# Kernel tuning notes

Hardware: AMD Instinct MI355X
Metric: run time of the kernel (lower is better)

The kernel has to match this reference:

```python
import jax, jax.numpy as jnp
import numpy as np

N_NODES = 100000
N_EDGES = 1600000
IN_FEATS, HIDDEN, OUT_MU, OUT_LV = 256, 128, 64, 64


def setup_inputs() -> dict:
    key = jax.random.key(0)
    ks = jax.random.split(key, 8)
    X = jax.random.normal(ks[0], (N_NODES, IN_FEATS), dtype=jnp.float32)
    edge_index = jax.random.randint(ks[1], (2, N_EDGES), 0, N_NODES, dtype=jnp.int64)
    def glorot(k, shape):
        lim = np.sqrt(6.0 / (shape[0] + shape[1])).astype(np.float32)
        return jax.random.uniform(k, shape, jnp.float32, -lim, lim)
    W1 = glorot(ks[2], (IN_FEATS, HIDDEN))
    b1 = jnp.zeros((HIDDEN,), jnp.float32)
    Wmu = glorot(ks[3], (HIDDEN, OUT_MU))
    bmu = jnp.zeros((OUT_MU,), jnp.float32)
    Wlv = glorot(ks[4], (HIDDEN, OUT_LV))
    blv = jnp.zeros((OUT_LV,), jnp.float32)
    return {"X": X, "edge_index": edge_index, "W1": W1, "b1": b1,
            "Wmu": Wmu, "bmu": bmu, "Wlv": Wlv, "blv": blv}


def _gcn_norm(edge_index, num_nodes):
    # Add self-loops (PyG GCNConv default) and compute symmetric normalization.
    loop = jnp.arange(num_nodes, dtype=edge_index.dtype)
    row = jnp.concatenate([edge_index[0], loop])  # source
    col = jnp.concatenate([edge_index[1], loop])  # target
    deg = jax.ops.segment_sum(jnp.ones_like(col, dtype=jnp.float32), col,
                              num_segments=num_nodes)
    dinv = jnp.where(deg > 0, jax.lax.rsqrt(deg), 0.0)
    norm = dinv[row] * dinv[col]  # [E+N]
    return row, col, norm


def _gcn_conv(x, W, b, row, col, norm, num_nodes):
    # Linear transform, then normalized sparse neighbor aggregation at targets.
    h = x @ W                                   # [N, F_out]
    msg = h[row] * norm[:, None]                # gather + scale, [E+N, F_out]
    out = jax.ops.segment_sum(msg, col, num_segments=num_nodes)
    return out + b


def reference(X, edge_index, W1, b1, Wmu, bmu, Wlv, blv):
    n = X.shape[0]
    row, col, norm = _gcn_norm(edge_index, n)
    H = jax.nn.relu(_gcn_conv(X, W1, b1, row, col, norm, n))
    mu = _gcn_conv(H, Wmu, bmu, row, col, norm, n)
    lv = _gcn_conv(H, Wlv, blv, row, col, norm, n)
    return (mu, lv)
```

## Files before the change

### kernel.cpp

```cpp
#include <hip/hip_runtime.h>
#include <hip/hip_bf16.h>
#include <cstdint>

#define N_FEATS_IN 256
#define HID 128
#define OUTF 64
#define NBMAX 400
#define BCAP 6144

typedef __bf16 bf16x8 __attribute__((ext_vector_type(8)));
typedef __bf16 bf16x4 __attribute__((ext_vector_type(4)));
typedef __bf16 bf16x2 __attribute__((ext_vector_type(2)));
typedef float f32x4 __attribute__((ext_vector_type(4)));



__global__ __launch_bounds__(256) void bucket_count(const int* __restrict__ ei, int E,
    int CH, int NB, int* __restrict__ gbk, int* __restrict__ bbase) {
  __shared__ int cnt[NBMAX];
  const int t = threadIdx.x, blk = blockIdx.x;
  for (int i = t; i < NB; i += 256) cnt[i] = 0;
  __syncthreads();
  int base = blk * CH, lim = min(base + CH, E);
  for (int i = base + t; i < lim; i += 256) atomicAdd(&cnt[ei[E + i] >> 8], 1);
  __syncthreads();
  for (int i = t; i < NB; i += 256) {
    int b = (i + blk) % NB;
    int v = cnt[b];
    bbase[(size_t)blk * NB + b] = (v > 0) ? atomicAdd(&gbk[b], v) : 0;
  }
}

__global__ __launch_bounds__(512) void bucket_scan(const int* __restrict__ gbk,
    int* __restrict__ gbkoff, int NB, int E) {
  __shared__ int ts[512];
  const int t = threadIdx.x;
  int v = (t < NB) ? gbk[t] : 0;
  ts[t] = v;
  __syncthreads();
  for (int off = 1; off < 512; off <<= 1) {
    int u = (t >= off) ? ts[t - off] : 0;
    __syncthreads();
    ts[t] += u;
    __syncthreads();
  }
  if (t < NB) gbkoff[t] = ts[t] - v;
  if (t == 0) gbkoff[NB] = E;
}

__global__ __launch_bounds__(256) void bucket_scatter(const int* __restrict__ ei, int E,
    int CH, int NB, const int* __restrict__ gbkoff, const int* __restrict__ bbase,
    int2* __restrict__ bucketed) {
  __shared__ int cur[NBMAX];
  const int t = threadIdx.x, blk = blockIdx.x;
  for (int i = t; i < NB; i += 256)
    cur[i] = gbkoff[i] + bbase[(size_t)blk * NB + i];
  __syncthreads();
  int base = blk * CH, lim = min(base + CH, E);
  for (int i = base + t; i < lim; i += 256) {
    int s = ei[i];
    int c = ei[E + i];
    int p = atomicAdd(&cur[c >> 8], 1);
    bucketed[p] = make_int2(s, c);
  }
}

__global__ __launch_bounds__(256) void bucket_csr(const int2* __restrict__ bucketed,
    const int* __restrict__ gbkoff, int NB, int N, int E,
    float* __restrict__ dinv, int* __restrict__ ptr, int* __restrict__ csrc) {
  __shared__ int2 eb[BCAP];
  __shared__ int cnt[256], scn[256], cur[256];
  const int b = blockIdx.x, t = threadIdx.x;
  const int beg = gbkoff[b], end = gbkoff[b + 1];
  const int M = end - beg;
  cnt[t] = 0;
  __syncthreads();
  const bool inlds = (M <= BCAP);
  if (inlds) {
    for (int i = t; i < M; i += 256) {
      int2 r = bucketed[beg + i];
      eb[i] = r;
      atomicAdd(&cnt[r.y & 255], 1);
    }
  } else {
    for (int i = t; i < M; i += 256) atomicAdd(&cnt[bucketed[beg + i].y & 255], 1);
  }
  __syncthreads();
  const int c0 = cnt[t];
  scn[t] = c0;
  __syncthreads();
  for (int off = 1; off < 256; off <<= 1) {
    int u = (t >= off) ? scn[t - off] : 0;
    __syncthreads();
    scn[t] += u;
    __syncthreads();
  }
  const int excl = scn[t] - c0;
  const int node = b * 256 + t;
  if (node < N) {
    ptr[node] = beg + excl;
    dinv[node] = rsqrtf((float)(c0 + 1));
  }
  if (b == NB - 1 && t == 0) ptr[N] = E;
  cur[t] = excl;
  __syncthreads();
  if (inlds) {
    for (int i = t; i < M; i += 256) {
      int2 r = eb[i];
      int slot = atomicAdd(&cur[r.y & 255], 1);
      csrc[beg + slot] = r.x;
    }
  } else {
    for (int i = t; i < M; i += 256) {
      int2 r = bucketed[beg + i];
      int slot = atomicAdd(&cur[r.y & 255], 1);
      csrc[beg + slot] = r.x;
    }
  }
}


__global__ __launch_bounds__(256) void pack_all_kernel(const float* __restrict__ W1,
    const float* __restrict__ Wmu, const float* __restrict__ Wlv,
    __bf16* __restrict__ W1p, __bf16* __restrict__ Wcp) {
  int idx = blockIdx.x * 256 + threadIdx.x;
  if (idx < 32768) {
    int j = idx & 7, l = (idx >> 3) & 63, t = (idx >> 9) & 7, s = idx >> 12;
    int k = s * 32 + (l >> 4) * 8 + j;
    int n = t * 16 + (l & 15);
    W1p[idx] = (__bf16)W1[k * HID + n];
  } else if (idx < 49152) {
    int i2 = idx - 32768;
    int j = i2 & 7, l = (i2 >> 3) & 63, t = (i2 >> 9) & 7, s = i2 >> 12;
    int k = s * 32 + (l >> 4) * 8 + j;
    int g = t * 16 + (l & 15);
    float v = (g < OUTF) ? Wmu[k * OUTF + g] : Wlv[k * OUTF + (g - OUTF)];
    Wcp[i2] = (__bf16)v;
  }
}


__global__ __launch_bounds__(256) void gemm1_mfma(const float* __restrict__ X,
    const __bf16* __restrict__ Wp, const float* __restrict__ dinv,
    __bf16* __restrict__ Yb, int nrows) {
  const int tid = threadIdx.x;
  const int lane = tid & 63;
  const int wave = tid >> 6;
  const int lm = lane & 15;
  const int q = lane >> 4;
  const int rowbase = blockIdx.x * 128 + wave * 32;

  const int r0 = min(rowbase + lm, nrows - 1);
  const int r1 = min(rowbase + 16 + lm, nrows - 1);
  const float* x0 = X + (size_t)r0 * N_FEATS_IN + q * 8;
  const float* x1 = X + (size_t)r1 * N_FEATS_IN + q * 8;

  const bf16x8* wp = (const bf16x8*)Wp;

  f32x4 acc[2][8];
#pragma unroll
  for (int m = 0; m < 2; ++m)
#pragma unroll
    for (int t = 0; t < 8; ++t) acc[m][t] = (f32x4)0.f;

#pragma unroll
  for (int s = 0; s < 8; ++s) {
    float4 l0 = *(const float4*)(x0 + s * 32);
    float4 h0 = *(const float4*)(x0 + s * 32 + 4);
    float4 l1 = *(const float4*)(x1 + s * 32);
    float4 h1 = *(const float4*)(x1 + s * 32 + 4);
    bf16x8 a0, a1;
    a0[0] = (__bf16)l0.x; a0[1] = (__bf16)l0.y; a0[2] = (__bf16)l0.z; a0[3] = (__bf16)l0.w;
    a0[4] = (__bf16)h0.x; a0[5] = (__bf16)h0.y; a0[6] = (__bf16)h0.z; a0[7] = (__bf16)h0.w;
    a1[0] = (__bf16)l1.x; a1[1] = (__bf16)l1.y; a1[2] = (__bf16)l1.z; a1[3] = (__bf16)l1.w;
    a1[4] = (__bf16)h1.x; a1[5] = (__bf16)h1.y; a1[6] = (__bf16)h1.z; a1[7] = (__bf16)h1.w;
#pragma unroll
    for (int t = 0; t < 8; ++t) {
      bf16x8 b = wp[(s * 8 + t) * 64 + lane];
      acc[0][t] = __builtin_amdgcn_mfma_f32_16x16x32_bf16(a0, b, acc[0][t], 0, 0, 0);
      acc[1][t] = __builtin_amdgcn_mfma_f32_16x16x32_bf16(a1, b, acc[1][t], 0, 0, 0);
    }
  }

  float dd[2][4];
#pragma unroll
  for (int m = 0; m < 2; ++m)
#pragma unroll
    for (int r2 = 0; r2 < 4; ++r2) {
      int row = rowbase + m * 16 + q * 4 + r2;
      dd[m][r2] = (row < nrows) ? dinv[row] : 0.f;
    }

#pragma unroll
  for (int m = 0; m < 2; ++m) {
    int rb = rowbase + m * 16 + q * 4;
#pragma unroll
    for (int t = 0; t < 8; ++t) {
      __bf16* yslice = Yb + (size_t)t * nrows * 16;
#pragma unroll
      for (int r2 = 0; r2 < 4; ++r2) {
        int row = rb + r2;
        if (row < nrows)
          yslice[(size_t)row * 16 + lm] = (__bf16)(acc[m][t][r2] * dd[m][r2]);
      }
    }
  }
}


__global__ __launch_bounds__(256) void agg_kernel(const __bf16* __restrict__ Fin,
    const int* __restrict__ ptr, const int* __restrict__ csrc,
    const float* __restrict__ dinv, const float* __restrict__ bias,
    __bf16* __restrict__ Fout, int do_relu, int N) {
  const int tid = threadIdx.x;
  const int s = blockIdx.x & 7;
  const int tb = blockIdx.x >> 3;
  const int g = tid >> 2;
  const int fl = tid & 3;
  const int c = tb * 64 + g;
  if (c >= N) return;

  const __bf16* F = Fin + (size_t)s * N * 16;
  const float d = dinv[c];
  bf16x4 sv = ((const bf16x4*)(F + (size_t)c * 16))[fl];
  float a0 = (float)sv[0], a1 = (float)sv[1], a2 = (float)sv[2], a3 = (float)sv[3];

  const int beg = ptr[c], end = ptr[c + 1];
  int e = beg;
  for (; e + 8 <= end; e += 8) {
    int r[8];
#pragma unroll
    for (int i = 0; i < 8; ++i) r[i] = csrc[e + i];
    bf16x4 v[8];
#pragma unroll
    for (int i = 0; i < 8; ++i) v[i] = ((const bf16x4*)(F + (size_t)r[i] * 16))[fl];
#pragma unroll
    for (int i = 0; i < 8; ++i) {
      a0 += (float)v[i][0];
      a1 += (float)v[i][1];
      a2 += (float)v[i][2];
      a3 += (float)v[i][3];
    }
  }
  for (; e < end; ++e) {
    int r = csrc[e];
    bf16x4 v = ((const bf16x4*)(F + (size_t)r * 16))[fl];
    a0 += (float)v[0];
    a1 += (float)v[1];
    a2 += (float)v[2];
    a3 += (float)v[3];
  }

  if (do_relu) {
    float4 bv = ((const float4*)bias)[s * 4 + fl];
    a0 = fmaxf(fmaf(d, a0, bv.x), 0.f) * d;
    a1 = fmaxf(fmaf(d, a1, bv.y), 0.f) * d;
    a2 = fmaxf(fmaf(d, a2, bv.z), 0.f) * d;
    a3 = fmaxf(fmaf(d, a3, bv.w), 0.f) * d;
  } else {
    a0 *= d; a1 *= d; a2 *= d; a3 *= d;
  }
  bf16x4 o;
  o[0] = (__bf16)a0; o[1] = (__bf16)a1; o[2] = (__bf16)a2; o[3] = (__bf16)a3;
  ((bf16x4*)(Fout + (size_t)s * N * 16 + (size_t)c * 16))[fl] = o;
}


__global__ __launch_bounds__(256) void gemm2_mfma(const __bf16* __restrict__ Gb,
    const __bf16* __restrict__ Wp, const float* __restrict__ bmu,
    const float* __restrict__ blv, float* __restrict__ out, int nrows, int ntiles) {
  __shared__ __bf16 bs[16384];
  const int tid = threadIdx.x;
  {
    const float4* s4 = (const float4*)Wp;
    float4* d4 = (float4*)bs;
#pragma unroll
    for (int i = 0; i < 8; ++i) d4[tid + 256 * i] = s4[tid + 256 * i];
  }
  __syncthreads();
  const int lane = tid & 63;
  const int wave = tid >> 6;
  const int lm = lane & 15;
  const int q = lane >> 4;
  const bf16x8* bsv = (const bf16x8*)bs;

  float bv[8];
  size_t obase[8];
#pragma unroll
  for (int t = 0; t < 8; ++t) {
    int col = t * 16 + lm;
    bv[t] = (col < OUTF) ? bmu[col] : blv[col - OUTF];
    obase[t] = (col < OUTF) ? (size_t)col : ((size_t)nrows * OUTF + (col - OUTF));
  }

  for (int tile = blockIdx.x; tile < ntiles; tile += gridDim.x) {
    const int row0 = tile * 64 + wave * 16;
    const int r = min(row0 + lm, nrows - 1);

    bf16x8 xa[4];
#pragma unroll
    for (int si = 0; si < 4; ++si) {
      int chunk = si * 4 + q;
      xa[si] = *(const bf16x8*)(Gb + (size_t)(chunk >> 1) * nrows * 16 +
                                (size_t)r * 16 + (chunk & 1) * 8);
    }

    f32x4 acc[8];
#pragma unroll
    for (int t = 0; t < 8; ++t) acc[t] = (f32x4)0.f;

#pragma unroll
    for (int si = 0; si < 4; ++si) {
#pragma unroll
      for (int t = 0; t < 8; ++t)
        acc[t] = __builtin_amdgcn_mfma_f32_16x16x32_bf16(xa[si], bsv[(si * 8 + t) * 64 + lane],
                                                         acc[t], 0, 0, 0);
    }
#pragma unroll
    for (int t = 0; t < 8; ++t) {
#pragma unroll
      for (int r2 = 0; r2 < 4; ++r2) {
        int row = row0 + q * 4 + r2;
        if (row < nrows) out[obase[t] + (size_t)row * OUTF] = acc[t][r2] + bv[t];
      }
    }
  }
}


extern "C" void kernel_launch(void* const* d_in, const int* in_sizes, int n_in,
                              void* d_out, int out_size, void* d_ws, size_t ws_size,
                              hipStream_t stream) {
  const float* X   = (const float*)d_in[0];
  const int*   ei  = (const int*)d_in[1];
  const float* W1  = (const float*)d_in[2];
  const float* b1  = (const float*)d_in[3];
  const float* Wmu = (const float*)d_in[4];
  const float* bmu = (const float*)d_in[5];
  const float* Wlv = (const float*)d_in[6];
  const float* blv = (const float*)d_in[7];
  float* out = (float*)d_out;

  const int N = in_sizes[0] / N_FEATS_IN;
  const int E = in_sizes[1] / 2;

  char* ws = (char*)d_ws;
  size_t off = 0;
  auto alloc = [&](size_t bytes) -> void* {
    void* p = ws + off;
    off += (bytes + 255) & ~(size_t)255;
    return p;
  };
  __bf16* Yb   = (__bf16*)alloc((size_t)N * HID * 2);
  __bf16* Hb   = (__bf16*)alloc((size_t)N * HID * 2);
  float* dinv  = (float*)alloc((size_t)N * 4);
  int*   ptr   = (int*)alloc((size_t)(N + 1) * 4);
  int2*  bucketed = (int2*)alloc((size_t)E * 8);
  int*   csrc  = (int*)alloc((size_t)E * 4);
  int*   gbk   = (int*)alloc((size_t)NBMAX * 4);
  int*   gbkoff = (int*)alloc((size_t)(NBMAX + 1) * 4);
  int*   bbase = (int*)alloc((size_t)256 * NBMAX * 4);
  __bf16* W1p  = (__bf16*)alloc(32768 * 2);
  __bf16* Wcp  = (__bf16*)alloc(16384 * 2);
  (void)ws_size; (void)n_in; (void)out_size;

  const int NB = (N + 255) >> 8;
  const int P = 256;
  const int CH = (E + P - 1) / P;

  hipMemsetAsync(gbk, 0, (size_t)NB * 4, stream);
  bucket_count<<<P, 256, 0, stream>>>(ei, E, CH, NB, gbk, bbase);
  bucket_scan<<<1, 512, 0, stream>>>(gbk, gbkoff, NB, E);
  bucket_scatter<<<P, 256, 0, stream>>>(ei, E, CH, NB, gbkoff, bbase, bucketed);
  bucket_csr<<<NB, 256, 0, stream>>>(bucketed, gbkoff, NB, N, E, dinv, ptr, csrc);
  pack_all_kernel<<<192, 256, 0, stream>>>(W1, Wmu, Wlv, W1p, Wcp);

  int g1 = (N + 127) / 128;
  gemm1_mfma<<<g1, 256, 0, stream>>>(X, W1p, dinv, Yb, N);
  int ga = ((N + 63) / 64) * 8;
  agg_kernel<<<ga, 256, 0, stream>>>(Yb, ptr, csrc, dinv, b1, Hb, 1, N);
  agg_kernel<<<ga, 256, 0, stream>>>(Hb, ptr, csrc, dinv, b1, Yb, 0, N);
  int ntiles2 = (N + 63) / 64;
  int g2 = ntiles2 < 768 ? ntiles2 : 768;
  gemm2_mfma<<<g2, 256, 0, stream>>>(Yb, Wcp, bmu, blv, out, N, ntiles2);
}
```

Baseline: 452.4 us.

## Sort nodes by in-degree to balance aggregation warps

Builds a degree-bucketed permutation of nodes (64 bins via a global histogram, scan, and scatter) during CSR construction, and has the aggregation kernels process nodes in that order. Nodes with similar degree then land in the same wavefront, reducing divergence from uneven neighbor loop lengths. In exchange it adds two small kernels, an extra memset, an indirection load per node, and loses the locality of consecutive node indices for the self-feature and output accesses.

After: 531.2 us. 1.17x slower.

```diff
diff --git a/kernel.cpp b/kernel.cpp
--- a/kernel.cpp
+++ b/kernel.cpp
@@ -7,6 +7,7 @@
 #define OUTF 64
 #define NBMAX 400
 #define BCAP 6144
+#define DBINS 64
 
 typedef __bf16 bf16x8 __attribute__((ext_vector_type(8)));
 typedef __bf16 bf16x4 __attribute__((ext_vector_type(4)));
@@ -67,13 +68,16 @@
 
 __global__ __launch_bounds__(256) void bucket_csr(const int2* __restrict__ bucketed,
     const int* __restrict__ gbkoff, int NB, int N, int E,
-    float* __restrict__ dinv, int* __restrict__ ptr, int* __restrict__ csrc) {
+    float* __restrict__ dinv, int* __restrict__ ptr, int* __restrict__ csrc,
+    int* __restrict__ dbing, int* __restrict__ noderank) {
   __shared__ int2 eb[BCAP];
   __shared__ int cnt[256], scn[256], cur[256];
+  __shared__ int dh[DBINS], dbase[DBINS];
   const int b = blockIdx.x, t = threadIdx.x;
   const int beg = gbkoff[b], end = gbkoff[b + 1];
   const int M = end - beg;
   cnt[t] = 0;
+  if (t < DBINS) dh[t] = 0;
   __syncthreads();
   const bool inlds = (M <= BCAP);
   if (inlds) {
@@ -97,13 +101,19 @@
   }
   const int excl = scn[t] - c0;
   const int node = b * 256 + t;
+  int bin = 0, lrk = 0;
   if (node < N) {
     ptr[node] = beg + excl;
     dinv[node] = rsqrtf((float)(c0 + 1));
+    bin = min(c0, DBINS - 1);
+    lrk = atomicAdd(&dh[bin], 1);
   }
   if (b == NB - 1 && t == 0) ptr[N] = E;
   cur[t] = excl;
   __syncthreads();
+  if (t < DBINS) dbase[t] = dh[t] ? atomicAdd(&dbing[t * 32], dh[t]) : 0;
+  __syncthreads();
+  if (node < N) noderank[node] = ((dbase[bin] + lrk) << 6) | bin;
   if (inlds) {
     for (int i = t; i < M; i += 256) {
       int2 r = eb[i];
@@ -116,6 +126,27 @@
       int slot = atomicAdd(&cur[r.y & 255], 1);
       csrc[beg + slot] = r.x;
     }
+  }
+}
+
+__global__ __launch_bounds__(64) void deg_scan(const int* __restrict__ dbing,
+    int* __restrict__ dboff) {
+  int t = threadIdx.x;
+  int v = dbing[t * 32];
+  int x = v;
+  for (int off = 1; off < 64; off <<= 1) {
+    int u = __shfl_up(x, off);
+    if (t >= off) x += u;
+  }
+  dboff[t] = x - v;
+}
+
+__global__ __launch_bounds__(256) void perm_scatter(const int* __restrict__ noderank,
+    const int* __restrict__ dboff, int* __restrict__ perm, int N) {
+  int i = blockIdx.x * 256 + threadIdx.x;
+  if (i < N) {
+    int w = noderank[i];
+    perm[dboff[w & 63] + (w >> 6)] = i;
   }
 }
 
@@ -211,14 +242,16 @@
 __global__ __launch_bounds__(256) void agg_kernel(const __bf16* __restrict__ Fin,
     const int* __restrict__ ptr, const int* __restrict__ csrc,
     const float* __restrict__ dinv, const float* __restrict__ bias,
+    const int* __restrict__ perm,
     __bf16* __restrict__ Fout, int do_relu, int N) {
   const int tid = threadIdx.x;
   const int s = blockIdx.x & 7;
   const int tb = blockIdx.x >> 3;
   const int g = tid >> 2;
   const int fl = tid & 3;
-  const int c = tb * 64 + g;
-  if (c >= N) return;
+  const int idx = tb * 64 + g;
+  if (idx >= N) return;
+  const int c = perm[idx];
 
   const __bf16* F = Fin + (size_t)s * N * 16;
   const float d = dinv[c];
@@ -360,6 +393,10 @@
   int*   gbk   = (int*)alloc((size_t)NBMAX * 4);
   int*   gbkoff = (int*)alloc((size_t)(NBMAX + 1) * 4);
   int*   bbase = (int*)alloc((size_t)256 * NBMAX * 4);
+  int*   dbing = (int*)alloc((size_t)DBINS * 32 * 4);
+  int*   dboff = (int*)alloc((size_t)DBINS * 4);
+  int*   noderank = (int*)alloc((size_t)N * 4);
+  int*   perm  = (int*)alloc((size_t)N * 4);
   __bf16* W1p  = (__bf16*)alloc(32768 * 2);
   __bf16* Wcp  = (__bf16*)alloc(16384 * 2);
   (void)ws_size; (void)n_in; (void)out_size;
@@ -369,17 +406,21 @@
   const int CH = (E + P - 1) / P;
 
   hipMemsetAsync(gbk, 0, (size_t)NB * 4, stream);
+  hipMemsetAsync(dbing, 0, (size_t)DBINS * 32 * 4, stream);
   bucket_count<<<P, 256, 0, stream>>>(ei, E, CH, NB, gbk, bbase);
   bucket_scan<<<1, 512, 0, stream>>>(gbk, gbkoff, NB, E);
   bucket_scatter<<<P, 256, 0, stream>>>(ei, E, CH, NB, gbkoff, bbase, bucketed);
-  bucket_csr<<<NB, 256, 0, stream>>>(bucketed, gbkoff, NB, N, E, dinv, ptr, csrc);
+  bucket_csr<<<NB, 256, 0, stream>>>(bucketed, gbkoff, NB, N, E, dinv, ptr, csrc,
+                                     dbing, noderank);
+  deg_scan<<<1, 64, 0, stream>>>(dbing, dboff);
+  perm_scatter<<<(N + 255) / 256, 256, 0, stream>>>(noderank, dboff, perm, N);
   pack_all_kernel<<<192, 256, 0, stream>>>(W1, Wmu, Wlv, W1p, Wcp);
 
   int g1 = (N + 127) / 128;
   gemm1_mfma<<<g1, 256, 0, stream>>>(X, W1p, dinv, Yb, N);
   int ga = ((N + 63) / 64) * 8;
-  agg_kernel<<<ga, 256, 0, stream>>>(Yb, ptr, csrc, dinv, b1, Hb, 1, N);
-  agg_kernel<<<ga, 256, 0, stream>>>(Hb, ptr, csrc, dinv, b1, Yb, 0, N);
+  agg_kernel<<<ga, 256, 0, stream>>>(Yb, ptr, csrc, dinv, b1, perm, Hb, 1, N);
+  agg_kernel<<<ga, 256, 0, stream>>>(Hb, ptr, csrc, dinv, b1, perm, Yb, 0, N);
   int ntiles2 = (N + 63) / 64;
   int g2 = ntiles2 < 768 ? ntiles2 : 768;
   gemm2_mfma<<<g2, 256, 0, stream>>>(Yb, Wcp, bmu, blv, out, N, ntiles2);
```

## Widen feature slices to 32 and pack bucketed edges into single words

Applied to the files above, without the earlier changes.

The bf16 feature slices move from 8 slices of 16 columns to 4 slices of 32 columns. This is applied consistently in gemm1's store, both aggregation passes and gemm2's load, so each gathered neighbour row becomes a 64-byte contiguous read and the aggregation grid has half as many slice passes. The aggregation now loads the 8 neighbour indices cooperatively, one per lane, and broadcasts them with shuffles instead of every lane reading all 8. Bucketed edges are packed into one 32-bit word (low 8 bits of the target in the top byte, source in the low 24 bits), halving that buffer's traffic. The packing assumes node ids fit in 24 bits.

Measured after the change: 430.1 us. 4.9% less time.

```diff
diff --git a/kernel.cpp b/kernel.cpp
--- a/kernel.cpp
+++ b/kernel.cpp
@@ -10,8 +10,8 @@
 
 typedef __bf16 bf16x8 __attribute__((ext_vector_type(8)));
 typedef __bf16 bf16x4 __attribute__((ext_vector_type(4)));
-typedef __bf16 bf16x2 __attribute__((ext_vector_type(2)));
 typedef float f32x4 __attribute__((ext_vector_type(4)));
+
 
 
 
@@ -50,7 +50,7 @@
 
 __global__ __launch_bounds__(256) void bucket_scatter(const int* __restrict__ ei, int E,
     int CH, int NB, const int* __restrict__ gbkoff, const int* __restrict__ bbase,
-    int2* __restrict__ bucketed) {
+    unsigned int* __restrict__ pk) {
   __shared__ int cur[NBMAX];
   const int t = threadIdx.x, blk = blockIdx.x;
   for (int i = t; i < NB; i += 256)
@@ -58,17 +58,17 @@
   __syncthreads();
   int base = blk * CH, lim = min(base + CH, E);
   for (int i = base + t; i < lim; i += 256) {
-    int s = ei[i];
+    unsigned int s = (unsigned int)ei[i];
     int c = ei[E + i];
     int p = atomicAdd(&cur[c >> 8], 1);
-    bucketed[p] = make_int2(s, c);
-  }
-}
-
-__global__ __launch_bounds__(256) void bucket_csr(const int2* __restrict__ bucketed,
+    pk[p] = ((unsigned int)(c & 255) << 24) | s;
+  }
+}
+
+__global__ __launch_bounds__(256) void bucket_csr(const unsigned int* __restrict__ pk,
     const int* __restrict__ gbkoff, int NB, int N, int E,
     float* __restrict__ dinv, int* __restrict__ ptr, int* __restrict__ csrc) {
-  __shared__ int2 eb[BCAP];
+  __shared__ unsigned int eb[BCAP];
   __shared__ int cnt[256], scn[256], cur[256];
   const int b = blockIdx.x, t = threadIdx.x;
   const int beg = gbkoff[b], end = gbkoff[b + 1];
@@ -78,12 +78,12 @@
   const bool inlds = (M <= BCAP);
   if (inlds) {
     for (int i = t; i < M; i += 256) {
-      int2 r = bucketed[beg + i];
+      unsigned int r = pk[beg + i];
       eb[i] = r;
-      atomicAdd(&cnt[r.y & 255], 1);
+      atomicAdd(&cnt[r >> 24], 1);
     }
   } else {
-    for (int i = t; i < M; i += 256) atomicAdd(&cnt[bucketed[beg + i].y & 255], 1);
+    for (int i = t; i < M; i += 256) atomicAdd(&cnt[pk[beg + i] >> 24], 1);
   }
   __syncthreads();
   const int c0 = cnt[t];
@@ -106,15 +106,15 @@
   __syncthreads();
   if (inlds) {
     for (int i = t; i < M; i += 256) {
-      int2 r = eb[i];
-      int slot = atomicAdd(&cur[r.y & 255], 1);
-      csrc[beg + slot] = r.x;
+      unsigned int r = eb[i];
+      int slot = atomicAdd(&cur[r >> 24], 1);
+      csrc[beg + slot] = (int)(r & 0xFFFFFFu);
     }
   } else {
     for (int i = t; i < M; i += 256) {
-      int2 r = bucketed[beg + i];
-      int slot = atomicAdd(&cur[r.y & 255], 1);
-      csrc[beg + slot] = r.x;
+      unsigned int r = pk[beg + i];
+      int slot = atomicAdd(&cur[r >> 24], 1);
+      csrc[beg + slot] = (int)(r & 0xFFFFFFu);
     }
   }
 }
@@ -196,12 +196,13 @@
     int rb = rowbase + m * 16 + q * 4;
 #pragma unroll
     for (int t = 0; t < 8; ++t) {
-      __bf16* yslice = Yb + (size_t)t * nrows * 16;
+      __bf16* yslice = Yb + (size_t)(t >> 1) * nrows * 32;
+      const int o = (t & 1) * 16 + lm;
 #pragma unroll
       for (int r2 = 0; r2 < 4; ++r2) {
         int row = rb + r2;
         if (row < nrows)
-          yslice[(size_t)row * 16 + lm] = (__bf16)(acc[m][t][r2] * dd[m][r2]);
+          yslice[(size_t)row * 32 + o] = (__bf16)(acc[m][t][r2] * dd[m][r2]);
       }
     }
   }
@@ -213,27 +214,30 @@
     const float* __restrict__ dinv, const float* __restrict__ bias,
     __bf16* __restrict__ Fout, int do_relu, int N) {
   const int tid = threadIdx.x;
-  const int s = blockIdx.x & 7;
-  const int tb = blockIdx.x >> 3;
-  const int g = tid >> 2;
-  const int fl = tid & 3;
-  const int c = tb * 64 + g;
+  const int s = blockIdx.x & 3;
+  const int tb = blockIdx.x >> 2;
+  const int g = tid >> 3;
+  const int fl = tid & 7;
+  const int lane = tid & 63;
+  const int c = tb * 32 + g;
   if (c >= N) return;
 
-  const __bf16* F = Fin + (size_t)s * N * 16;
+  const __bf16* F = Fin + (size_t)s * N * 32;
   const float d = dinv[c];
-  bf16x4 sv = ((const bf16x4*)(F + (size_t)c * 16))[fl];
+  bf16x4 sv = ((const bf16x4*)(F + (size_t)c * 32))[fl];
   float a0 = (float)sv[0], a1 = (float)sv[1], a2 = (float)sv[2], a3 = (float)sv[3];
 
   const int beg = ptr[c], end = ptr[c + 1];
+  const int gbase = lane & 56;
   int e = beg;
   for (; e + 8 <= end; e += 8) {
+    int rown = csrc[e + fl];
     int r[8];
 #pragma unroll
-    for (int i = 0; i < 8; ++i) r[i] = csrc[e + i];
+    for (int i = 0; i < 8; ++i) r[i] = __shfl(rown, gbase | i);
     bf16x4 v[8];
 #pragma unroll
-    for (int i = 0; i < 8; ++i) v[i] = ((const bf16x4*)(F + (size_t)r[i] * 16))[fl];
+    for (int i = 0; i < 8; ++i) v[i] = ((const bf16x4*)(F + (size_t)r[i] * 32))[fl];
 #pragma unroll
     for (int i = 0; i < 8; ++i) {
       a0 += (float)v[i][0];
@@ -244,7 +248,7 @@
   }
   for (; e < end; ++e) {
     int r = csrc[e];
-    bf16x4 v = ((const bf16x4*)(F + (size_t)r * 16))[fl];
+    bf16x4 v = ((const bf16x4*)(F + (size_t)r * 32))[fl];
     a0 += (float)v[0];
     a1 += (float)v[1];
     a2 += (float)v[2];
@@ -252,7 +256,7 @@
   }
 
   if (do_relu) {
-    float4 bv = ((const float4*)bias)[s * 4 + fl];
+    float4 bv = ((const float4*)bias)[s * 8 + fl];
     a0 = fmaxf(fmaf(d, a0, bv.x), 0.f) * d;
     a1 = fmaxf(fmaf(d, a1, bv.y), 0.f) * d;
     a2 = fmaxf(fmaf(d, a2, bv.z), 0.f) * d;
@@ -262,7 +266,7 @@
   }
   bf16x4 o;
   o[0] = (__bf16)a0; o[1] = (__bf16)a1; o[2] = (__bf16)a2; o[3] = (__bf16)a3;
-  ((bf16x4*)(Fout + (size_t)s * N * 16 + (size_t)c * 16))[fl] = o;
+  ((bf16x4*)(Fout + (size_t)s * N * 32 + (size_t)c * 32))[fl] = o;
 }
 
 
@@ -301,8 +305,8 @@
 #pragma unroll
     for (int si = 0; si < 4; ++si) {
       int chunk = si * 4 + q;
-      xa[si] = *(const bf16x8*)(Gb + (size_t)(chunk >> 1) * nrows * 16 +
-                                (size_t)r * 16 + (chunk & 1) * 8);
+      xa[si] = *(const bf16x8*)(Gb + (size_t)(chunk >> 2) * nrows * 32 +
+                                (size_t)r * 32 + (chunk & 3) * 8);
     }
 
     f32x4 acc[8];
@@ -355,7 +359,7 @@
   __bf16* Hb   = (__bf16*)alloc((size_t)N * HID * 2);
   float* dinv  = (float*)alloc((size_t)N * 4);
   int*   ptr   = (int*)alloc((size_t)(N + 1) * 4);
-  int2*  bucketed = (int2*)alloc((size_t)E * 8);
+  unsigned int* pk = (unsigned int*)alloc((size_t)E * 4);
   int*   csrc  = (int*)alloc((size_t)E * 4);
   int*   gbk   = (int*)alloc((size_t)NBMAX * 4);
   int*   gbkoff = (int*)alloc((size_t)(NBMAX + 1) * 4);
@@ -371,13 +375,13 @@
   hipMemsetAsync(gbk, 0, (size_t)NB * 4, stream);
   bucket_count<<<P, 256, 0, stream>>>(ei, E, CH, NB, gbk, bbase);
   bucket_scan<<<1, 512, 0, stream>>>(gbk, gbkoff, NB, E);
-  bucket_scatter<<<P, 256, 0, stream>>>(ei, E, CH, NB, gbkoff, bbase, bucketed);
-  bucket_csr<<<NB, 256, 0, stream>>>(bucketed, gbkoff, NB, N, E, dinv, ptr, csrc);
+  bucket_scatter<<<P, 256, 0, stream>>>(ei, E, CH, NB, gbkoff, bbase, pk);
+  bucket_csr<<<NB, 256, 0, stream>>>(pk, gbkoff, NB, N, E, dinv, ptr, csrc);
   pack_all_kernel<<<192, 256, 0, stream>>>(W1, Wmu, Wlv, W1p, Wcp);
 
   int g1 = (N + 127) / 128;
   gemm1_mfma<<<g1, 256, 0, stream>>>(X, W1p, dinv, Yb, N);
-  int ga = ((N + 63) / 64) * 8;
+  int ga = ((N + 31) / 32) * 4;
   agg_kernel<<<ga, 256, 0, stream>>>(Yb, ptr, csrc, dinv, b1, Hb, 1, N);
   agg_kernel<<<ga, 256, 0, stream>>>(Hb, ptr, csrc, dinv, b1, Yb, 0, N);
   int ntiles2 = (N + 63) / 64;
```
